# Optimization experiments

Hardware: AMD Instinct MI355X
Metric: run time of the kernel (lower is better)

The kernel has to match this reference:

```python
import jax, jax.numpy as jnp
import numpy as np


def setup_inputs() -> dict:
    key = jax.random.key(0)
    k1, k2 = jax.random.split(key)
    B, A, H, W, C = 4, 9, 256, 256, 9
    F = 64
    lfi = jax.random.normal(k1, (B, A, H, W, C), dtype=jnp.float32)
    f_maps = jax.random.uniform(k2, (B, H, W, F), dtype=jnp.float32)
    return {"lfi": lfi, "f_maps": f_maps}


def reference(lfi, f_maps):
    # height mask: per (b, filter), mean of the [h,w] map over rows, normalized by its max.
    # f_maps: [B, H, W, F] -> hv: [B, W, F]; note original asserts W == H.
    hv = jnp.mean(f_maps, axis=1)                      # [B, W, F]
    hv = hv / jnp.max(hv, axis=1, keepdims=True)       # normalize per (b, f)
    h_mask = jnp.transpose(hv, (0, 2, 1))              # [B, F, H]
    # lfi: [B, A, H, W, C]; h_feat[b,f] = lfi[b] * h_mask[b,f,:] broadcast over H axis,
    # then mean over angular dims A and C -> factorizes as mean(lfi) * h_mask.
    m = jnp.mean(lfi, axis=(1, 4))                     # [B, H, W]
    out = jnp.einsum('bhw,bfh->bhwf', m, h_mask)       # [B, H, W, F]
    return out
```

## Files before the change

kernel.cpp:

```cpp
#include <hip/hip_runtime.h>

#define BB 4
#define AA 9
#define HH 256
#define WW 256
#define CC 9
#define FF 64

__global__ __launch_bounds__(256) void k_hv(const float* __restrict__ fm,
                                            float* __restrict__ hv) {
    const int blk = blockIdx.x;
    const int b = blk >> 8;
    const int w = blk & 255;
    const int f = threadIdx.x & 63;
    const int hl = threadIdx.x >> 6;

    const float* base = fm + (((size_t)b * HH) * WW + w) * FF + f;
    float s = 0.f;
#pragma unroll 8
    for (int h = hl; h < HH; h += 4) {
        s += base[(size_t)h * WW * FF];
    }
    __shared__ float sm[256];
    sm[threadIdx.x] = s;
    __syncthreads();
    if (hl == 0) {
        float t = sm[f] + sm[64 + f] + sm[128 + f] + sm[192 + f];
        hv[(size_t)blk * FF + f] = t * (1.0f / HH);
    }
}

__global__ __launch_bounds__(64) void k_inv(const float* __restrict__ hv,
                                            float* __restrict__ inv) {
    const int b = blockIdx.x >> 6;
    const int f = blockIdx.x & 63;
    const int t = threadIdx.x;
    float mx = -1e30f;
#pragma unroll
    for (int j = 0; j < 4; ++j) {
        mx = fmaxf(mx, hv[((size_t)b * WW + (t + 64 * j)) * FF + f]);
    }
#pragma unroll
    for (int off = 32; off; off >>= 1)
        mx = fmaxf(mx, __shfl_xor(mx, off));
    if (t == 0) inv[blockIdx.x] = 1.0f / mx;
}

__global__ __launch_bounds__(256) void k_m(const float* __restrict__ lfi,
                                           float* __restrict__ m) {
    const int gid = blockIdx.x * 256 + threadIdx.x;
    const int b = gid >> 16;
    const int hw = gid & 65535;

    const size_t astride = (size_t)HH * WW * CC;
    const float* base = lfi + (size_t)b * AA * astride + (size_t)hw * CC;

    float s = 0.f;
#pragma unroll
    for (int a = 0; a < AA; ++a) {
        const float* p = base + (size_t)a * astride;
#pragma unroll
        for (int c = 0; c < CC; ++c) s += p[c];
    }
    m[gid] = s * (1.0f / (AA * CC));
}

__global__ __launch_bounds__(256) void k_out(const float* __restrict__ m,
                                             const float* __restrict__ hv,
                                             const float* __restrict__ inv,
                                             float4* __restrict__ out) {
    const int idx = blockIdx.x * 256 + threadIdx.x;
    const int f4 = idx & 15;
    const int rest = idx >> 4;
    const int h = (rest >> 8) & 255;
    const int b = rest >> 16;

    const float mv = m[rest];
    const float4 hv4 = ((const float4*)hv)[((size_t)(b * HH + h)) * (FF / 4) + f4];
    const float4 iv4 = ((const float4*)inv)[b * (FF / 4) + f4];

    float4 o;
    o.x = mv * hv4.x * iv4.x;
    o.y = mv * hv4.y * iv4.y;
    o.z = mv * hv4.z * iv4.z;
    o.w = mv * hv4.w * iv4.w;
    out[idx] = o;
}

extern "C" void kernel_launch(void* const* d_in, const int* in_sizes, int n_in,
                              void* d_out, int out_size, void* d_ws, size_t ws_size,
                              hipStream_t stream) {
    const float* lfi = (const float*)d_in[0];
    const float* fm  = (const float*)d_in[1];
    float* out = (float*)d_out;

    char* ws = (char*)d_ws;
    float* hv  = (float*)ws;
    float* inv = (float*)(ws + (size_t)BB * WW * FF * 4);
    float* m   = (float*)(ws + (size_t)BB * WW * FF * 4 + 1024);

    k_hv<<<BB * WW, 256, 0, stream>>>(fm, hv);
    k_inv<<<BB * FF, 64, 0, stream>>>(hv, inv);
    k_m<<<(BB * HH * WW) / 256, 256, 0, stream>>>(lfi, m);
    k_out<<<(BB * HH * WW * FF / 4) / 256, 256, 0, stream>>>(m, hv, inv, (float4*)out);
}
```

Baseline: 44.27 us.

## Merge hv and m reductions into one kernel with atomic max normalization

Fuses the column-mean reduction over f_maps and the angular mean over lfi into a single launch by splitting the grid between the two jobs. It replaces the separate max kernel with an integer atomicMax on the float bits, cleared by a memset first, and vectorizes the f_maps loads as float4. The integer trick assumes the means are non-negative, which holds because f_maps is uniform. The output kernel now divides by the max instead of multiplying by a precomputed reciprocal, trading launch overhead for per-element divides.

```diff
diff --git a/kernel.cpp b/kernel.cpp
--- a/kernel.cpp
+++ b/kernel.cpp
@@ -7,67 +7,60 @@
 #define CC 9
 #define FF 64
 
-__global__ __launch_bounds__(256) void k_hv(const float* __restrict__ fm,
-                                            float* __restrict__ hv) {
-    const int blk = blockIdx.x;
-    const int b = blk >> 8;
-    const int w = blk & 255;
-    const int f = threadIdx.x & 63;
-    const int hl = threadIdx.x >> 6;
+__global__ __launch_bounds__(256) void k_stage1(const float* __restrict__ fm,
+                                                const float* __restrict__ lfi,
+                                                float* __restrict__ hv,
+                                                int* __restrict__ maxbuf,
+                                                float* __restrict__ m) {
+    if (blockIdx.x < BB * WW) {
+        const int blk = blockIdx.x;
+        const int b = blk >> 8;
+        const int w = blk & 255;
+        const int f4 = threadIdx.x & 15;
+        const int hl = threadIdx.x >> 4;
 
-    const float* base = fm + (((size_t)b * HH) * WW + w) * FF + f;
-    float s = 0.f;
-#pragma unroll 8
-    for (int h = hl; h < HH; h += 4) {
-        s += base[(size_t)h * WW * FF];
+        const float4* base =
+            (const float4*)fm + (((size_t)b * HH) * WW + w) * (FF / 4) + f4;
+        float4 acc = make_float4(0.f, 0.f, 0.f, 0.f);
+#pragma unroll
+        for (int h = hl; h < HH; h += 16) {
+            float4 v = base[(size_t)h * WW * (FF / 4)];
+            acc.x += v.x; acc.y += v.y; acc.z += v.z; acc.w += v.w;
+        }
+        __shared__ float sm[16 * FF];
+        ((float4*)sm)[hl * 16 + f4] = acc;
+        __syncthreads();
+        if (threadIdx.x < FF) {
+            const int f = threadIdx.x;
+            float t = 0.f;
+#pragma unroll
+            for (int j = 0; j < 16; ++j) t += sm[j * FF + f];
+            t *= (1.0f / HH);
+            hv[(size_t)blk * FF + f] = t;
+            atomicMax(maxbuf + b * FF + f, __float_as_int(t));
+        }
+    } else {
+        const int gid = (blockIdx.x - BB * WW) * 256 + threadIdx.x;
+        const int b = gid >> 16;
+        const int hw = gid & 65535;
+
+        const size_t astride = (size_t)HH * WW * CC;
+        const float* base = lfi + (size_t)b * AA * astride + (size_t)hw * CC;
+
+        float s = 0.f;
+#pragma unroll
+        for (int a = 0; a < AA; ++a) {
+            const float* p = base + (size_t)a * astride;
+#pragma unroll
+            for (int c = 0; c < CC; ++c) s += p[c];
+        }
+        m[gid] = s * (1.0f / (AA * CC));
     }
-    __shared__ float sm[256];
-    sm[threadIdx.x] = s;
-    __syncthreads();
-    if (hl == 0) {
-        float t = sm[f] + sm[64 + f] + sm[128 + f] + sm[192 + f];
-        hv[(size_t)blk * FF + f] = t * (1.0f / HH);
-    }
-}
-
-__global__ __launch_bounds__(64) void k_inv(const float* __restrict__ hv,
-                                            float* __restrict__ inv) {
-    const int b = blockIdx.x >> 6;
-    const int f = blockIdx.x & 63;
-    const int t = threadIdx.x;
-    float mx = -1e30f;
-#pragma unroll
-    for (int j = 0; j < 4; ++j) {
-        mx = fmaxf(mx, hv[((size_t)b * WW + (t + 64 * j)) * FF + f]);
-    }
-#pragma unroll
-    for (int off = 32; off; off >>= 1)
-        mx = fmaxf(mx, __shfl_xor(mx, off));
-    if (t == 0) inv[blockIdx.x] = 1.0f / mx;
-}
-
-__global__ __launch_bounds__(256) void k_m(const float* __restrict__ lfi,
-                                           float* __restrict__ m) {
-    const int gid = blockIdx.x * 256 + threadIdx.x;
-    const int b = gid >> 16;
-    const int hw = gid & 65535;
-
-    const size_t astride = (size_t)HH * WW * CC;
-    const float* base = lfi + (size_t)b * AA * astride + (size_t)hw * CC;
-
-    float s = 0.f;
-#pragma unroll
-    for (int a = 0; a < AA; ++a) {
-        const float* p = base + (size_t)a * astride;
-#pragma unroll
-        for (int c = 0; c < CC; ++c) s += p[c];
-    }
-    m[gid] = s * (1.0f / (AA * CC));
 }
 
 __global__ __launch_bounds__(256) void k_out(const float* __restrict__ m,
                                              const float* __restrict__ hv,
-                                             const float* __restrict__ inv,
+                                             const int* __restrict__ maxbuf,
                                              float4* __restrict__ out) {
     const int idx = blockIdx.x * 256 + threadIdx.x;
     const int f4 = idx & 15;
@@ -77,13 +70,13 @@
 
     const float mv = m[rest];
     const float4 hv4 = ((const float4*)hv)[((size_t)(b * HH + h)) * (FF / 4) + f4];
-    const float4 iv4 = ((const float4*)inv)[b * (FF / 4) + f4];
+    const int4 mx4 = ((const int4*)maxbuf)[b * (FF / 4) + f4];
 
     float4 o;
-    o.x = mv * hv4.x * iv4.x;
-    o.y = mv * hv4.y * iv4.y;
-    o.z = mv * hv4.z * iv4.z;
-    o.w = mv * hv4.w * iv4.w;
+    o.x = mv * hv4.x / __int_as_float(mx4.x);
+    o.y = mv * hv4.y / __int_as_float(mx4.y);
+    o.z = mv * hv4.z / __int_as_float(mx4.z);
+    o.w = mv * hv4.w / __int_as_float(mx4.w);
     out[idx] = o;
 }
 
@@ -96,11 +89,10 @@
 
     char* ws = (char*)d_ws;
     float* hv  = (float*)ws;
-    float* inv = (float*)(ws + (size_t)BB * WW * FF * 4);
+    int*   mxb = (int*)(ws + (size_t)BB * WW * FF * 4);
     float* m   = (float*)(ws + (size_t)BB * WW * FF * 4 + 1024);
 
-    k_hv<<<BB * WW, 256, 0, stream>>>(fm, hv);
-    k_inv<<<BB * FF, 64, 0, stream>>>(hv, inv);
-    k_m<<<(BB * HH * WW) / 256, 256, 0, stream>>>(lfi, m);
-    k_out<<<(BB * HH * WW * FF / 4) / 256, 256, 0, stream>>>(m, hv, inv, (float4*)out);
+    hipMemsetAsync(mxb, 0, BB * FF * sizeof(int), stream);
+    k_stage1<<<BB * WW + (BB * HH * WW) / 256, 256, 0, stream>>>(fm, lfi, hv, mxb, m);
+    k_out<<<(BB * HH * WW * FF / 4) / 256, 256, 0, stream>>>(m, hv, mxb, (float4*)out);
 }
```

Measured after the change: 47.83 us. 1.08x slower.

## Vectorize lfi reduction with float4 loads and split angular sum three ways

Applied to the files above, without the earlier changes.

The per-pixel angular/channel mean kernel now has each thread load contiguous float4 runs covering four pixels' 9 channels, replacing strided scalar loads. The A dimension is split across three block roles that write partial sums, and the output kernel adds the three partials and applies the normalization. This aims to improve memory coalescing and give more parallelism on the largest input read. In exchange, it adds three partial-buffer reads per output element and a larger workspace.

```diff
diff --git a/kernel.cpp b/kernel.cpp
--- a/kernel.cpp
+++ b/kernel.cpp
@@ -46,26 +46,33 @@
     if (t == 0) inv[blockIdx.x] = 1.0f / mx;
 }
 
-__global__ __launch_bounds__(256) void k_m(const float* __restrict__ lfi,
-                                           float* __restrict__ m) {
-    const int gid = blockIdx.x * 256 + threadIdx.x;
-    const int b = gid >> 16;
-    const int hw = gid & 65535;
+__global__ __launch_bounds__(256) void k_m3(const float* __restrict__ lfi,
+                                            float* __restrict__ mpart) {
+    const int t = threadIdx.x;
+    const int role = blockIdx.x >> 8;
+    const int hw4 = (blockIdx.x & 255) * 256 + t;
+    const int b = hw4 >> 14;
+    const int hwl = (hw4 & 16383) * 4;
+    const size_t astride4 = (size_t)HH * WW * CC / 4;
 
-    const size_t astride = (size_t)HH * WW * CC;
-    const float* base = lfi + (size_t)b * AA * astride + (size_t)hw * CC;
-
-    float s = 0.f;
+    const float4* base =
+        (const float4*)(lfi + (size_t)b * AA * (astride4 * 4)) +
+        (size_t)hwl * CC / 4;
+    float4 acc = make_float4(0.f, 0.f, 0.f, 0.f);
 #pragma unroll
-    for (int a = 0; a < AA; ++a) {
-        const float* p = base + (size_t)a * astride;
-#pragma unroll
-        for (int c = 0; c < CC; ++c) s += p[c];
+    for (int a = role * 3; a < role * 3 + 3; ++a) {
+        const float4* p = base + (size_t)a * astride4;
+        float4 v0 = p[0], v1 = p[1], v2 = p[2], v3 = p[3], v4 = p[4];
+        float4 v5 = p[5], v6 = p[6], v7 = p[7], v8 = p[8];
+        acc.x += v0.x + v0.y + v0.z + v0.w + v1.x + v1.y + v1.z + v1.w + v2.x;
+        acc.y += v2.y + v2.z + v2.w + v3.x + v3.y + v3.z + v3.w + v4.x + v4.y;
+        acc.z += v4.z + v4.w + v5.x + v5.y + v5.z + v5.w + v6.x + v6.y + v6.z;
+        acc.w += v6.w + v7.x + v7.y + v7.z + v7.w + v8.x + v8.y + v8.z + v8.w;
     }
-    m[gid] = s * (1.0f / (AA * CC));
+    ((float4*)mpart)[(size_t)role * 65536 + hw4] = acc;
 }
 
-__global__ __launch_bounds__(256) void k_out(const float* __restrict__ m,
+__global__ __launch_bounds__(256) void k_out(const float* __restrict__ mpart,
                                              const float* __restrict__ hv,
                                              const float* __restrict__ inv,
                                              float4* __restrict__ out) {
@@ -75,7 +82,8 @@
     const int h = (rest >> 8) & 255;
     const int b = rest >> 16;
 
-    const float mv = m[rest];
+    const float mv = (mpart[rest] + mpart[262144 + rest] +
+                      mpart[524288 + rest]) * (1.0f / (AA * CC));
     const float4 hv4 = ((const float4*)hv)[((size_t)(b * HH + h)) * (FF / 4) + f4];
     const float4 iv4 = ((const float4*)inv)[b * (FF / 4) + f4];
 
@@ -95,12 +103,13 @@
     float* out = (float*)d_out;
 
     char* ws = (char*)d_ws;
-    float* hv  = (float*)ws;
-    float* inv = (float*)(ws + (size_t)BB * WW * FF * 4);
-    float* m   = (float*)(ws + (size_t)BB * WW * FF * 4 + 1024);
+    float* hv   = (float*)ws;
+    float* inv  = (float*)(ws + (size_t)BB * WW * FF * 4);
+    float* mprt = (float*)(ws + (size_t)BB * WW * FF * 4 + 4096);
 
     k_hv<<<BB * WW, 256, 0, stream>>>(fm, hv);
     k_inv<<<BB * FF, 64, 0, stream>>>(hv, inv);
-    k_m<<<(BB * HH * WW) / 256, 256, 0, stream>>>(lfi, m);
-    k_out<<<(BB * HH * WW * FF / 4) / 256, 256, 0, stream>>>(m, hv, inv, (float4*)out);
+    k_m3<<<3 * 256, 256, 0, stream>>>(lfi, mprt);
+    k_out<<<(BB * HH * WW * FF / 4) / 256, 256, 0, stream>>>(mprt, hv, inv,
+                                                             (float4*)out);
 }
```

After: 50.06 us. +13.1%, slower.
